# Performance work log

Hardware: AMD Instinct MI355X
Metric: run time of the kernel (lower is better)

Reference implementation:

```python
import jax, jax.numpy as jnp
import numpy as np
import math

D_MODEL, D_INNER, D_STATE, D_CONV, DT_RANK = 768, 1536, 16, 4, 48
BATCH, SEQLEN = 2, 1024
DT_MIN, DT_MAX = 1e-4, 1.0


def setup_inputs() -> dict:
    key = jax.random.key(0)
    ks = jax.random.split(key, 10)
    D, N, R, K = D_INNER, D_STATE, DT_RANK, D_CONV
    total_out = 2 * D + R + 2 * D * N

    def xavier(k, shape):
        fan_in, fan_out = shape[1], shape[0]
        a = math.sqrt(6.0 / (fan_in + fan_out))
        return jax.random.uniform(k, shape, jnp.float32, -a, a)

    x = jax.random.normal(ks[0], (BATCH, SEQLEN, D_MODEL), jnp.float32)
    W_in = xavier(ks[1], (total_out, D_MODEL))
    W_dt = xavier(ks[2], (D, R))
    W_out = xavier(ks[3], (D_MODEL, D))
    W_res = xavier(ks[4], (D, D_MODEL))
    conv_w = jax.random.normal(ks[5], (D, K), jnp.float32) * (1.0 / math.sqrt(K))
    conv_b = jnp.zeros((D,), jnp.float32)
    # A_log init: log(1..N) per inner channel
    A_log = jnp.broadcast_to(jnp.log(jnp.arange(1, N + 1, dtype=jnp.float32)), (D, N))
    Dskip = jnp.ones((D,), jnp.float32)
    # dt_bias = inverse_softplus(exp(uniform in [log dt_min, log dt_max]))
    dt = jnp.exp(jax.random.uniform(ks[6], (D,), jnp.float32) * (math.log(DT_MAX) - math.log(DT_MIN)) + math.log(DT_MIN))
    dt_bias = dt + jnp.log(-jnp.expm1(-dt))
    norm_w = jnp.ones((D,), jnp.float32)
    ln_w = jnp.ones((D_MODEL,), jnp.float32)
    ln_b = jnp.zeros((D_MODEL,), jnp.float32)
    return {
        "x": x, "ln_w": ln_w, "ln_b": ln_b, "W_in": W_in, "W_dt": W_dt,
        "conv_w": conv_w, "conv_b": conv_b, "A_log": A_log, "Dskip": Dskip,
        "dt_bias": dt_bias, "norm_w": norm_w, "W_res": W_res, "W_out": W_out,
    }


def _forward(x, ln_w, ln_b, W_in, W_dt, conv_w, conv_b, A_log, Dskip, dt_bias, norm_w, W_res, W_out):
    B, L, _ = x.shape
    D, N = A_log.shape
    K = conv_w.shape[1]
    R = W_dt.shape[1]
    # pre LayerNorm
    mu = x.mean(-1, keepdims=True)
    var = ((x - mu) ** 2).mean(-1, keepdims=True)
    xn = (x - mu) * jax.lax.rsqrt(var + 1e-5) * ln_w + ln_b
    # fused input projection, then split
    p = jnp.einsum('bld,od->blo', xn, W_in)  # (B,L,2D+R+2DN)
    z = p[..., :D]
    u = p[..., D:2 * D]
    dth = p[..., 2 * D:2 * D + R]
    Bpar = p[..., 2 * D + R:2 * D + R + D * N].reshape(B, L, D, N)
    Cpar = p[..., 2 * D + R + D * N:].reshape(B, L, D, N)
    # causal depthwise conv over time on u
    uc = jax.lax.conv_general_dilated(
        u.transpose(0, 2, 1), conv_w[:, None, :], (1,), [(K - 1, 0)],
        feature_group_count=D, dimension_numbers=('NCH', 'OIH', 'NCH'))
    u = (uc + conv_b[None, :, None]).transpose(0, 2, 1)  # (B,L,D)
    # dt: low-rank proj + bias -> softplus -> clamp
    dt = jnp.clip(jax.nn.softplus(jnp.einsum('blr,dr->bld', dth, W_dt) + dt_bias), DT_MIN, DT_MAX)
    A = -jnp.exp(A_log)  # (D,N), negative
    dA = jnp.exp(dt[..., None] * A)          # (B,L,D,N)
    dBu = (dt * u)[..., None] * Bpar         # (B,L,D,N)

    def step(h, inp):
        dA_t, dBu_t, C_t = inp               # each (B,D,N)
        h = dA_t * h + dBu_t
        return h, (C_t * h).sum(-1)          # y_t: (B,D)

    h0 = jnp.zeros((B, D, N), x.dtype)
    _, ys = jax.lax.scan(step, h0, (dA.transpose(1, 0, 2, 3),
                                    dBu.transpose(1, 0, 2, 3),
                                    Cpar.transpose(1, 0, 2, 3)))
    y = ys.transpose(1, 0, 2) + u * Dskip    # (B,L,D)
    # fused gated RMSNorm + inner residual
    res = jnp.einsum('blm,dm->bld', x, W_res)
    g = y * jax.nn.silu(z)
    g = g * jax.lax.rsqrt((g * g).mean(-1, keepdims=True) + 1e-6) * norm_w + res
    return jnp.einsum('bld,md->blm', g, W_out)


def reference(x, ln_w, ln_b, W_in, W_dt, conv_w, conv_b, A_log, Dskip, dt_bias, norm_w, W_res, W_out):
    return _forward(x, ln_w, ln_b, W_in, W_dt, conv_w, conv_b, A_log, Dskip, dt_bias, norm_w, W_res, W_out)
```

## Files before the change

### kernel.cpp

```cpp
#include <hip/hip_runtime.h>


typedef unsigned short u16;
typedef __bf16 bf16x8 __attribute__((ext_vector_type(8)));
typedef float f32x4 __attribute__((ext_vector_type(4)));

#define OPAD 52480
#define OTOT 52272
#define DI   1536
#define DM   768
#define Z0   0
#define U0   1536
#define DTH0 3072
#define B0   3120
#define C0   27696

#define SCAN_P 64
#define SCAN_T 16
#define SPF    4

#define LOG2E 1.442695040888963f

__device__ static inline u16 f2bf(float f) {
    unsigned u = __float_as_uint(f);
    u += 0x7fffu + ((u >> 16) & 1u);
    return (u16)(u >> 16);
}
__device__ static inline float bf2f(u16 s) {
    return __uint_as_float(((unsigned)s) << 16);
}

__device__ static inline void gload16(const void* g, void* l) {
    __builtin_amdgcn_global_load_lds(
        (const __attribute__((address_space(1))) unsigned int*)g,
        (__attribute__((address_space(3))) unsigned int*)l, 16, 0, 0);
}

__device__ static inline void unpack8(uint4 v, float* f) {
    unsigned w0 = v.x, w1 = v.y, w2 = v.z, w3 = v.w;
    f[0] = __uint_as_float(w0 << 16); f[1] = __uint_as_float(w0 & 0xffff0000u);
    f[2] = __uint_as_float(w1 << 16); f[3] = __uint_as_float(w1 & 0xffff0000u);
    f[4] = __uint_as_float(w2 << 16); f[5] = __uint_as_float(w2 & 0xffff0000u);
    f[6] = __uint_as_float(w3 << 16); f[7] = __uint_as_float(w3 & 0xffff0000u);
}

__device__ static inline void block_reduce2(float& a, float& b) {
    #pragma unroll
    for (int o = 32; o > 0; o >>= 1) {
        a += __shfl_down(a, o);
        b += __shfl_down(b, o);
    }
    __shared__ float sa[4], sb[4];
    int lane = threadIdx.x & 63, w = threadIdx.x >> 6;
    if (lane == 0) { sa[w] = a; sb[w] = b; }
    __syncthreads();
    a = sa[0] + sa[1] + sa[2] + sa[3];
    b = sb[0] + sb[1] + sb[2] + sb[3];
}

__global__ void __launch_bounds__(256) prep_kernel(
        const float* __restrict__ W_in, const float* __restrict__ W_res,
        const float* __restrict__ W_out, const float* __restrict__ x,
        const float* __restrict__ lnw, const float* __restrict__ lnb,
        u16* __restrict__ Wbf, u16* __restrict__ Wresbf, u16* __restrict__ Woutbf,
        u16* __restrict__ xnbf, u16* __restrict__ xbf) {
    int bid = blockIdx.x, tid = threadIdx.x;
    if (bid < 41664) {
        const float* src; u16* dst; long n_src, n_tot; long lb;
        if (bid < 39360) {
            src = W_in; dst = Wbf; n_src = (long)OTOT * DM; n_tot = (long)OPAD * DM;
            lb = bid;
        } else if (bid < 40512) {
            src = W_res; dst = Wresbf; n_src = (long)DI * DM; n_tot = n_src;
            lb = bid - 39360;
        } else {
            src = W_out; dst = Woutbf; n_src = (long)DM * DI; n_tot = n_src;
            lb = bid - 40512;
        }
        long i4 = (lb * 256 + tid) * 4;
        if (i4 >= n_tot) return;
        ushort4 o;
        if (i4 < n_src) {
            float4 v = *(const float4*)(src + i4);
            o.x = f2bf(v.x); o.y = f2bf(v.y); o.z = f2bf(v.z); o.w = f2bf(v.w);
        } else {
            o.x = o.y = o.z = o.w = 0;
        }
        *(ushort4*)(dst + i4) = o;
    } else {
        int m = bid - 41664;
        const float* xr = x + (size_t)m * DM;
        float v[3];
        v[0] = xr[tid]; v[1] = xr[tid + 256]; v[2] = xr[tid + 512];
        float s = v[0] + v[1] + v[2];
        float ss = v[0]*v[0] + v[1]*v[1] + v[2]*v[2];
        block_reduce2(s, ss);
        float mu = s * (1.f / DM);
        float var = ss * (1.f / DM) - mu * mu;
        float inv = rsqrtf(var + 1e-5f);
        #pragma unroll
        for (int i = 0; i < 3; ++i) {
            int d = tid + i * 256;
            float xn = (v[i] - mu) * inv * lnw[d] + lnb[d];
            xnbf[(size_t)m * DM + d] = f2bf(xn);
            xbf[(size_t)m * DM + d] = f2bf(v[i]);
        }
    }
}

template <int OUT_BF16, int ATOMIC>
__global__ void __launch_bounds__(256) gemm_bt(const u16* __restrict__ A,
        const u16* __restrict__ B, void* __restrict__ C, int K, int ldk, int ldc) {
    __shared__ u16 smem[2 * 128 * 64];
    u16* As = smem;
    u16* Bs = smem + 128 * 64;
    int tid = threadIdx.x;
    int m0 = blockIdx.x * 128, n0 = blockIdx.y * 128;
    int lane = tid & 63, wave = tid >> 6;
    int wm = wave >> 1, wn = wave & 1;
    int l15 = lane & 15, l4 = lane >> 4;
    f32x4 acc[4][4] = {};
    const u16* Ag = A + (size_t)m0 * ldk + (size_t)blockIdx.z * K;
    const u16* Bg = B + (size_t)n0 * ldk + (size_t)blockIdx.z * K;
    int crow = tid >> 3;
    int ccol = ((tid & 7) ^ ((tid >> 3) & 7)) * 8;
    int ldsoff = (tid & 192) * 16;
    int xr = l15 & 7;

    for (int k0 = 0; k0 < K; k0 += 64) {
        __syncthreads();
        #pragma unroll
        for (int it = 0; it < 4; ++it) {
            gload16(Ag + (size_t)(it * 32 + crow) * ldk + k0 + ccol,
                    (char*)As + it * 4096 + ldsoff);
            gload16(Bg + (size_t)(it * 32 + crow) * ldk + k0 + ccol,
                    (char*)Bs + it * 4096 + ldsoff);
        }
        __syncthreads();
        const u16* Arow = As + (wm * 64 + l15) * 64;
        const u16* Brow = Bs + (wn * 64 + l15) * 64;
        #pragma unroll
        for (int kk8 = 0; kk8 < 8; kk8 += 4) {
            int sw = ((l4 + kk8) ^ xr) * 8;
            bf16x8 af[4], bfr[4];
            #pragma unroll
            for (int i = 0; i < 4; ++i) af[i] = *(const bf16x8*)(Arow + i * 16 * 64 + sw);
            #pragma unroll
            for (int j = 0; j < 4; ++j) bfr[j] = *(const bf16x8*)(Brow + j * 16 * 64 + sw);
            #pragma unroll
            for (int i = 0; i < 4; ++i)
                #pragma unroll
                for (int j = 0; j < 4; ++j)
                    acc[i][j] = __builtin_amdgcn_mfma_f32_16x16x32_bf16(
                        af[i], bfr[j], acc[i][j], 0, 0, 0);
        }
    }
    #pragma unroll
    for (int i = 0; i < 4; ++i) {
        int row = m0 + wm * 64 + i * 16 + l4 * 4;
        #pragma unroll
        for (int j = 0; j < 4; ++j) {
            int col = n0 + wn * 64 + j * 16 + l15;
            #pragma unroll
            for (int r = 0; r < 4; ++r) {
                size_t off = (size_t)(row + r) * ldc + col;
                if (ATOMIC)        atomicAdd((float*)C + off, acc[i][j][r]);
                else if (OUT_BF16) ((u16*)C)[off] = f2bf(acc[i][j][r]);
                else               ((float*)C)[off] = acc[i][j][r];
            }
        }
    }
}

#define G2_BUF  65536
#define G2_HALF 16384
#define G2_BOFF 32768

__global__ void __launch_bounds__(512, 2) gemm256_bt(const u16* __restrict__ A,
        const u16* __restrict__ B, u16* __restrict__ C, int K, int ldc) {
    __shared__ u16 smem[65536];
    char* smemc = (char*)smem;
    const int tid = threadIdx.x;
    const int l = tid & 63, w = tid >> 6;
    const int wm = w >> 2, wn = w & 3;
    const int l15 = l & 15, l4 = l >> 4;
    const int flat = blockIdx.y * 8 + blockIdx.x;
    const int wg = (flat & 7) * 205 + (flat >> 3);
    const int m0 = (wg & 7) * 256, n0 = (wg >> 3) * 256;
    const int NT = K >> 6;

    const int rA = l15 >> 1;
    const int rdoff = rA * 128 + ((((l4 << 1) + (l15 & 1)) ^ ((rA & 3) << 1)) << 4);
    const int wpr = (l & 7) ^ (((l >> 3) & 3) << 1);
    const int srow = w * 32 + ((l >> 3) << 1) + (wpr & 1);
    const u16* Ast = A + (size_t)(m0 + srow) * K + (wpr >> 1) * 8;
    const u16* Bst = B + (size_t)(n0 + srow) * K + (wpr >> 1) * 8;
    const int sdst = w * 2048;

    f32x4 acc[8][4] = {};
    bf16x8 bvK[4];

#define G2_STAGE(MATP, MOFF, nxt, sh, tk)                                      \
    gload16(MATP + (size_t)(tk) * 64 + (sh) * 32,                              \
            smemc + (nxt) * G2_BUF + (MOFF) + (sh) * G2_HALF + sdst);          \
    gload16(MATP + (size_t)16 * K + (size_t)(tk) * 64 + (sh) * 32,             \
            smemc + (nxt) * G2_BUF + (MOFF) + (sh) * G2_HALF + sdst + 1024);

#define G2_PHASE(cur, nxt, rh, h, READB, SMAT, SMOFF, sh, tk, DO_VM)           \
    {                                                                          \
        G2_STAGE(SMAT, SMOFF, nxt, sh, tk);                                    \
        const char* Ab = smemc + (cur) * G2_BUF + (h) * G2_HALF                \
                         + (wm * 128 + (rh) * 64) * 64 + rdoff;                \
        bf16x8 af[4];                                                          \
        if (READB) {                                                           \
            const char* Bb = smemc + (cur) * G2_BUF + G2_BOFF + (h) * G2_HALF  \
                             + (wn * 64) * 64 + rdoff;                         \
            _Pragma("unroll")                                                  \
            for (int j = 0; j < 4; ++j)                                        \
                bvK[j] = *(const bf16x8*)(Bb + j * 1024);                      \
        }                                                                      \
        _Pragma("unroll")                                                      \
        for (int i = 0; i < 4; ++i) af[i] = *(const bf16x8*)(Ab + i * 1024);   \
        __builtin_amdgcn_s_barrier();                                          \
        __builtin_amdgcn_s_setprio(1);                                         \
        _Pragma("unroll")                                                      \
        for (int i = 0; i < 4; ++i)                                            \
            _Pragma("unroll")                                                  \
            for (int j = 0; j < 4; ++j)                                        \
                acc[(rh) * 4 + i][j] = __builtin_amdgcn_mfma_f32_16x16x32_bf16(\
                    af[i], bvK[j], acc[(rh) * 4 + i][j], 0, 0, 0);             \
        __builtin_amdgcn_s_setprio(0);                                         \
        if (DO_VM) asm volatile("s_waitcnt vmcnt(4)" ::: "memory");            \
        __builtin_amdgcn_s_barrier();                                          \
    }

#define G2_TILE(cur, nxt, tk)                                                  \
    G2_PHASE(cur, nxt, 0, 0, 1, Ast, 0,       0, tk, 0)                        \
    G2_PHASE(cur, nxt, 1, 0, 0, Bst, G2_BOFF, 0, tk, 1)                        \
    G2_PHASE(cur, nxt, 0, 1, 1, Ast, 0,       1, tk, 0)                        \
    G2_PHASE(cur, nxt, 1, 1, 0, Bst, G2_BOFF, 1, tk, 1)

    G2_STAGE(Ast, 0,       0, 0, 0);
    G2_STAGE(Bst, G2_BOFF, 0, 0, 0);
    G2_STAGE(Ast, 0,       0, 1, 0);
    G2_STAGE(Bst, G2_BOFF, 0, 1, 0);
    asm volatile("s_waitcnt vmcnt(4)" ::: "memory");
    __builtin_amdgcn_s_barrier();

    for (int t = 0; t < NT; t += 2) {
        int tk1 = t + 1;
        int tk2 = (t + 2 < NT) ? t + 2 : NT - 1;
        G2_TILE(0, 1, tk1)
        G2_TILE(1, 0, tk2)
    }

    #pragma unroll
    for (int ai = 0; ai < 8; ++ai) {
        int row = m0 + wm * 128 + ai * 16 + l4 * 4;
        #pragma unroll
        for (int j = 0; j < 4; ++j) {
            int col = n0 + wn * 64 + j * 16 + l15;
            #pragma unroll
            for (int r = 0; r < 4; ++r)
                C[(size_t)(row + r) * ldc + col] = f2bf(acc[ai][j][r]);
        }
    }
#undef G2_STAGE
#undef G2_PHASE
#undef G2_TILE
}

__global__ void __launch_bounds__(256) dt_kernel(const u16* __restrict__ p,
        const float* __restrict__ Wdt, const float* __restrict__ dt_bias,
        float* __restrict__ dt) {
    int m0 = blockIdx.x * 4, tid = threadIdx.x;
    __shared__ float dth_s[4 * 48];
    for (int i = tid; i < 4 * 48; i += 256)
        dth_s[i] = bf2f(p[(size_t)(m0 + i / 48) * OPAD + DTH0 + (i % 48)]);
    __syncthreads();
    #pragma unroll
    for (int ii = 0; ii < 6; ++ii) {
        int d = ii * 256 + tid;
        float base = dt_bias[d];
        float acc[4];
        #pragma unroll
        for (int mm = 0; mm < 4; ++mm) acc[mm] = base;
        for (int r = 0; r < 48; ++r) {
            float wv = Wdt[d * 48 + r];
            #pragma unroll
            for (int mm = 0; mm < 4; ++mm)
                acc[mm] = fmaf(wv, dth_s[mm * 48 + r], acc[mm]);
        }
        #pragma unroll
        for (int mm = 0; mm < 4; ++mm) {
            float xv = acc[mm];
            float sp = xv > 20.f ? xv : log1pf(__expf(xv));
            sp = fminf(fmaxf(sp, 1e-4f), 1.0f);
            dt[(size_t)(m0 + mm) * DI + d] = sp;
        }
    }
}

__global__ void __launch_bounds__(256, 2) scan1_kernel(const u16* __restrict__ p,
        const float* __restrict__ dt, const float* __restrict__ A_log,
        const float* __restrict__ cw, const float* __restrict__ cb,
        float* __restrict__ chkA, float* __restrict__ chkB) {
    int d = blockIdx.x * 256 + threadIdx.x;
    int b = blockIdx.y, c = blockIdx.z;
    int t0base = c * SCAN_T;
    float a[16];
    #pragma unroll
    for (int n = 0; n < 16; ++n) a[n] = -__expf(A_log[d * 16 + n]) * LOG2E;
    float cw0 = cw[d*4], cw1 = cw[d*4+1], cw2 = cw[d*4+2], cw3 = cw[d*4+3];
    float cbv = cb[d];
    const u16* pB = p + (size_t)(b * 1024 + t0base) * OPAD + B0 + d * 16;
    const u16* pU = p + (size_t)(b * 1024 + t0base) * OPAD + U0 + d;
    const float* dtp = dt + (size_t)(b * 1024 + t0base) * DI + d;
    float x1, x2, x3;
    if (c == 0) { x1 = x2 = x3 = 0.f; }
    else {
        x1 = bf2f(*(pU - (long)OPAD));
        x2 = bf2f(*(pU - 2L * OPAD));
        x3 = bf2f(*(pU - 3L * OPAD));
    }
    uint4 Br[SPF][2]; float dtr[SPF], xur[SPF];
    #pragma unroll
    for (int i = 0; i < SPF; ++i) {
        Br[i][0] = *(const uint4*)(pB + (size_t)i * OPAD);
        Br[i][1] = *(const uint4*)(pB + (size_t)i * OPAD + 8);
        dtr[i] = dtp[(size_t)i * DI];
        xur[i] = bf2f(pU[(size_t)i * OPAD]);
    }
    float h[16], Av[16];
    #pragma unroll
    for (int n = 0; n < 16; ++n) { h[n] = 0.f; Av[n] = 1.f; }
    for (int t0 = 0; t0 < SCAN_T; t0 += SPF) {
        #pragma unroll
        for (int s = 0; s < SPF; ++s) {
            int t = t0 + s;
            uint4 b0 = Br[s][0], b1 = Br[s][1];
            float dtv = dtr[s], xt = xur[s];
            int tl = t + SPF < SCAN_T ? t + SPF : SCAN_T - 1;
            Br[s][0] = *(const uint4*)(pB + (size_t)tl * OPAD);
            Br[s][1] = *(const uint4*)(pB + (size_t)tl * OPAD + 8);
            dtr[s] = dtp[(size_t)tl * DI];
            xur[s] = bf2f(pU[(size_t)tl * OPAD]);
            float uv = cbv;
            uv = fmaf(cw0, x3, uv);
            uv = fmaf(cw1, x2, uv);
            uv = fmaf(cw2, x1, uv);
            uv = fmaf(cw3, xt, uv);
            x3 = x2; x2 = x1; x1 = xt;
            float Bf[16];
            unpack8(b0, Bf); unpack8(b1, Bf + 8);
            float dtu = dtv * uv;
            #pragma unroll
            for (int n = 0; n < 16; ++n) {
                float dA = exp2f(dtv * a[n]);
                h[n] = fmaf(dA, h[n], dtu * Bf[n]);
                Av[n] *= dA;
            }
        }
    }
    size_t o = (((size_t)c * 2 + b) * 1536 + d) * 16;
    #pragma unroll
    for (int k = 0; k < 4; ++k) {
        *(float4*)(chkA + o + k * 4) = make_float4(Av[4*k], Av[4*k+1], Av[4*k+2], Av[4*k+3]);
        *(float4*)(chkB + o + k * 4) = make_float4(h[4*k], h[4*k+1], h[4*k+2], h[4*k+3]);
    }
}

__global__ void __launch_bounds__(256) scan_comb_kernel(const float* __restrict__ chkA,
        const float* __restrict__ chkB, float* __restrict__ hstart) {
    int idx = blockIdx.x * 256 + threadIdx.x;
    float hs = 0.f;
    for (int c = 0; c < SCAN_P; ++c) {
        size_t o = (size_t)c * 49152 + idx;
        hstart[o] = hs;
        hs = fmaf(chkA[o], hs, chkB[o]);
    }
}

__global__ void __launch_bounds__(256, 2) scan2_kernel(const u16* __restrict__ p,
        const float* __restrict__ dt, const float* __restrict__ A_log,
        const float* __restrict__ cw, const float* __restrict__ cb,
        const float* __restrict__ Dskip,
        const float* __restrict__ hstart, float* __restrict__ y) {
    int d = blockIdx.x * 256 + threadIdx.x;
    int b = blockIdx.y, c = blockIdx.z;
    int t0base = c * SCAN_T;
    float a[16];
    #pragma unroll
    for (int n = 0; n < 16; ++n) a[n] = -__expf(A_log[d * 16 + n]) * LOG2E;
    float Dsk = Dskip[d];
    float cw0 = cw[d*4], cw1 = cw[d*4+1], cw2 = cw[d*4+2], cw3 = cw[d*4+3];
    float cbv = cb[d];
    const u16* pB = p + (size_t)(b * 1024 + t0base) * OPAD + B0 + d * 16;
    const u16* pC = p + (size_t)(b * 1024 + t0base) * OPAD + C0 + d * 16;
    const u16* pU = p + (size_t)(b * 1024 + t0base) * OPAD + U0 + d;
    const float* dtp = dt + (size_t)(b * 1024 + t0base) * DI + d;
    float* yp        = y  + (size_t)(b * 1024 + t0base) * DI + d;
    float x1, x2, x3;
    if (c == 0) { x1 = x2 = x3 = 0.f; }
    else {
        x1 = bf2f(*(pU - (long)OPAD));
        x2 = bf2f(*(pU - 2L * OPAD));
        x3 = bf2f(*(pU - 3L * OPAD));
    }
    uint4 Br[SPF][2], Cr[SPF][2]; float dtr[SPF], xur[SPF];
    #pragma unroll
    for (int i = 0; i < SPF; ++i) {
        Br[i][0] = *(const uint4*)(pB + (size_t)i * OPAD);
        Br[i][1] = *(const uint4*)(pB + (size_t)i * OPAD + 8);
        Cr[i][0] = *(const uint4*)(pC + (size_t)i * OPAD);
        Cr[i][1] = *(const uint4*)(pC + (size_t)i * OPAD + 8);
        dtr[i] = dtp[(size_t)i * DI];
        xur[i] = bf2f(pU[(size_t)i * OPAD]);
    }
    float h[16];
    {
        size_t o = ((size_t)c * 3072 + (size_t)b * 1536 + d) * 16;
        #pragma unroll
        for (int k = 0; k < 4; ++k) {
            float4 hv = *(const float4*)(hstart + o + k * 4);
            h[4*k] = hv.x; h[4*k+1] = hv.y; h[4*k+2] = hv.z; h[4*k+3] = hv.w;
        }
    }
    for (int t0 = 0; t0 < SCAN_T; t0 += SPF) {
        #pragma unroll
        for (int s = 0; s < SPF; ++s) {
            int t = t0 + s;
            uint4 b0 = Br[s][0], b1 = Br[s][1], c0 = Cr[s][0], c1 = Cr[s][1];
            float dtv = dtr[s], xt = xur[s];
            int tl = t + SPF < SCAN_T ? t + SPF : SCAN_T - 1;
            Br[s][0] = *(const uint4*)(pB + (size_t)tl * OPAD);
            Br[s][1] = *(const uint4*)(pB + (size_t)tl * OPAD + 8);
            Cr[s][0] = *(const uint4*)(pC + (size_t)tl * OPAD);
            Cr[s][1] = *(const uint4*)(pC + (size_t)tl * OPAD + 8);
            dtr[s] = dtp[(size_t)tl * DI];
            xur[s] = bf2f(pU[(size_t)tl * OPAD]);
            float uv = cbv;
            uv = fmaf(cw0, x3, uv);
            uv = fmaf(cw1, x2, uv);
            uv = fmaf(cw2, x1, uv);
            uv = fmaf(cw3, xt, uv);
            x3 = x2; x2 = x1; x1 = xt;
            float Bf[16], Cf[16];
            unpack8(b0, Bf); unpack8(b1, Bf + 8);
            unpack8(c0, Cf); unpack8(c1, Cf + 8);
            float dtu = dtv * uv;
            #pragma unroll
            for (int n = 0; n < 16; ++n) {
                float dA = exp2f(dtv * a[n]);
                h[n] = fmaf(dA, h[n], dtu * Bf[n]);
            }
            float a0 = fmaf(Cf[0], h[0], uv * Dsk), a1 = Cf[1] * h[1];
            float a2 = Cf[2] * h[2], a3 = Cf[3] * h[3];
            #pragma unroll
            for (int n = 4; n < 16; n += 4) {
                a0 = fmaf(Cf[n],   h[n],   a0);
                a1 = fmaf(Cf[n+1], h[n+1], a1);
                a2 = fmaf(Cf[n+2], h[n+2], a2);
                a3 = fmaf(Cf[n+3], h[n+3], a3);
            }
            yp[(size_t)t * DI] = (a0 + a1) + (a2 + a3);
        }
    }
}

__global__ void __launch_bounds__(256) gate_kernel(const u16* __restrict__ p,
        const float* __restrict__ y, const float* __restrict__ res,
        const float* __restrict__ norm_w, u16* __restrict__ g) {
    int m = blockIdx.x, tid = threadIdx.x;
    const u16* pz = p + (size_t)m * OPAD + Z0;
    const float* yr = y + (size_t)m * DI;
    float gp[6];
    float ss = 0.f, dummy = 0.f;
    #pragma unroll
    for (int i = 0; i < 6; ++i) {
        int d = i * 256 + tid;
        float z = bf2f(pz[d]);
        float gv = yr[d] * z / (1.f + __expf(-z));
        gp[i] = gv;
        ss += gv * gv;
    }
    block_reduce2(ss, dummy);
    float scale = rsqrtf(ss * (1.f / DI) + 1e-6f);
    #pragma unroll
    for (int i = 0; i < 6; ++i) {
        int d = i * 256 + tid;
        float val = gp[i] * scale * norm_w[d] + res[(size_t)m * DI + d];
        g[(size_t)m * DI + d] = f2bf(val);
    }
}

extern "C" void kernel_launch(void* const* d_in, const int* in_sizes, int n_in,
                              void* d_out, int out_size, void* d_ws, size_t ws_size,
                              hipStream_t stream) {
    const float* x       = (const float*)d_in[0];
    const float* ln_w    = (const float*)d_in[1];
    const float* ln_b    = (const float*)d_in[2];
    const float* W_in    = (const float*)d_in[3];
    const float* W_dt    = (const float*)d_in[4];
    const float* conv_w  = (const float*)d_in[5];
    const float* conv_b  = (const float*)d_in[6];
    const float* A_log   = (const float*)d_in[7];
    const float* Dskip   = (const float*)d_in[8];
    const float* dt_bias = (const float*)d_in[9];
    const float* norm_w  = (const float*)d_in[10];
    const float* W_res   = (const float*)d_in[11];
    const float* W_out   = (const float*)d_in[12];
    float* out = (float*)d_out;

    char* wsb = (char*)d_ws;
    u16* Wbf     = (u16*)(wsb + 0);
    u16* Wresbf  = (u16*)(wsb + 80609280);
    u16* Woutbf  = (u16*)(wsb + 82968576);
    u16* xnbf    = (u16*)(wsb + 85327872);
    u16* xbf     = (u16*)(wsb + 88473600);
    u16* pbuf    = (u16*)(wsb + 91619328);
    float* dtv   = (float*)(wsb + 319160320);
    float* ybuf  = (float*)(wsb + 331743232);
    float* resb  = (float*)(wsb + 344326144);
    u16* gbuf    = (u16*)(wsb + 356909056);
    float* chkA  = (float*)(wsb + 0);
    float* chkB  = (float*)(wsb + 12582912);
    float* hst   = (float*)(wsb + 25165824);

    prep_kernel<<<43712, 256, 0, stream>>>(W_in, W_res, W_out, x, ln_w, ln_b,
                                           Wbf, Wresbf, Woutbf, xnbf, xbf);
    gemm256_bt<<<dim3(8, 205), 512, 0, stream>>>(xnbf, Wbf, pbuf, DM, OPAD);
    hipMemsetAsync(resb, 0, 12582912, stream);
    gemm_bt<0, 1><<<dim3(16, 12, 2), 256, 0, stream>>>(xbf, Wresbf, resb, 384, DM, DI);
    dt_kernel<<<512, 256, 0, stream>>>(pbuf, W_dt, dt_bias, dtv);
    scan1_kernel<<<dim3(6, 2, SCAN_P), 256, 0, stream>>>(pbuf, dtv, A_log, conv_w, conv_b, chkA, chkB);
    scan_comb_kernel<<<192, 256, 0, stream>>>(chkA, chkB, hst);
    scan2_kernel<<<dim3(6, 2, SCAN_P), 256, 0, stream>>>(pbuf, dtv, A_log, conv_w, conv_b, Dskip, hst, ybuf);
    gate_kernel<<<2048, 256, 0, stream>>>(pbuf, ybuf, resb, norm_w, gbuf);
    hipMemsetAsync(out, 0, (size_t)2048 * DM * 4, stream);
    gemm_bt<0, 1><<<dim3(16, 6, 4), 256, 0, stream>>>(gbuf, Woutbf, out, 384, DI, DM);
}
```

Before: 693.9 us.

## Fuse residual GEMM into main projection launch and drop split-K atomics

The residual projection x·W_res now runs as extra workgroups appended to the big input-projection GEMM launch. Each of these 512-thread blocks holds two independent 128x128 tiles over the full K=768 and stores fp32 directly, so the memset and atomic split-K path go away. The output projection also drops split-K: it runs 96 blocks over the full K with plain stores, removing a memset and the atomics. The cost is fewer blocks and therefore less parallelism on the output GEMM, plus uneven work inside the fused launch.

```diff
diff --git a/kernel.cpp b/kernel.cpp
--- a/kernel.cpp
+++ b/kernel.cpp
@@ -108,9 +108,9 @@
     }
 }
 
-template <int OUT_BF16, int ATOMIC>
+template <int OUT_BF16>
 __global__ void __launch_bounds__(256) gemm_bt(const u16* __restrict__ A,
-        const u16* __restrict__ B, void* __restrict__ C, int K, int ldk, int ldc) {
+        const u16* __restrict__ B, void* __restrict__ C, int K, int ldc) {
     __shared__ u16 smem[2 * 128 * 64];
     u16* As = smem;
     u16* Bs = smem + 128 * 64;
@@ -120,8 +120,8 @@
     int wm = wave >> 1, wn = wave & 1;
     int l15 = lane & 15, l4 = lane >> 4;
     f32x4 acc[4][4] = {};
-    const u16* Ag = A + (size_t)m0 * ldk + (size_t)blockIdx.z * K;
-    const u16* Bg = B + (size_t)n0 * ldk + (size_t)blockIdx.z * K;
+    const u16* Ag = A + (size_t)m0 * K;
+    const u16* Bg = B + (size_t)n0 * K;
     int crow = tid >> 3;
     int ccol = ((tid & 7) ^ ((tid >> 3) & 7)) * 8;
     int ldsoff = (tid & 192) * 16;
@@ -131,9 +131,9 @@
         __syncthreads();
         #pragma unroll
         for (int it = 0; it < 4; ++it) {
-            gload16(Ag + (size_t)(it * 32 + crow) * ldk + k0 + ccol,
+            gload16(Ag + (size_t)(it * 32 + crow) * K + k0 + ccol,
                     (char*)As + it * 4096 + ldsoff);
-            gload16(Bg + (size_t)(it * 32 + crow) * ldk + k0 + ccol,
+            gload16(Bg + (size_t)(it * 32 + crow) * K + k0 + ccol,
                     (char*)Bs + it * 4096 + ldsoff);
         }
         __syncthreads();
@@ -164,9 +164,8 @@
             #pragma unroll
             for (int r = 0; r < 4; ++r) {
                 size_t off = (size_t)(row + r) * ldc + col;
-                if (ATOMIC)        atomicAdd((float*)C + off, acc[i][j][r]);
-                else if (OUT_BF16) ((u16*)C)[off] = f2bf(acc[i][j][r]);
-                else               ((float*)C)[off] = acc[i][j][r];
+                if (OUT_BF16) ((u16*)C)[off] = f2bf(acc[i][j][r]);
+                else          ((float*)C)[off] = acc[i][j][r];
             }
         }
     }
@@ -177,28 +176,32 @@
 #define G2_BOFF 32768
 
 __global__ void __launch_bounds__(512, 2) gemm256_bt(const u16* __restrict__ A,
-        const u16* __restrict__ B, u16* __restrict__ C, int K, int ldc) {
+        const u16* __restrict__ B, u16* __restrict__ C, int K, int ldc,
+        const u16* __restrict__ Ares, const u16* __restrict__ Bres,
+        float* __restrict__ Cres) {
     __shared__ u16 smem[65536];
     char* smemc = (char*)smem;
     const int tid = threadIdx.x;
-    const int l = tid & 63, w = tid >> 6;
-    const int wm = w >> 2, wn = w & 3;
-    const int l15 = l & 15, l4 = l >> 4;
-    const int flat = blockIdx.y * 8 + blockIdx.x;
-    const int wg = (flat & 7) * 205 + (flat >> 3);
-    const int m0 = (wg & 7) * 256, n0 = (wg >> 3) * 256;
-    const int NT = K >> 6;
-
-    const int rA = l15 >> 1;
-    const int rdoff = rA * 128 + ((((l4 << 1) + (l15 & 1)) ^ ((rA & 3) << 1)) << 4);
-    const int wpr = (l & 7) ^ (((l >> 3) & 3) << 1);
-    const int srow = w * 32 + ((l >> 3) << 1) + (wpr & 1);
-    const u16* Ast = A + (size_t)(m0 + srow) * K + (wpr >> 1) * 8;
-    const u16* Bst = B + (size_t)(n0 + srow) * K + (wpr >> 1) * 8;
-    const int sdst = w * 2048;
-
-    f32x4 acc[8][4] = {};
-    bf16x8 bvK[4];
+    const int flat = blockIdx.x;
+
+    if (flat < 1640) {
+        const int l = tid & 63, w = tid >> 6;
+        const int wm = w >> 2, wn = w & 3;
+        const int l15 = l & 15, l4 = l >> 4;
+        const int wg = (flat & 7) * 205 + (flat >> 3);
+        const int m0 = (wg & 7) * 256, n0 = (wg >> 3) * 256;
+        const int NT = K >> 6;
+
+        const int rA = l15 >> 1;
+        const int rdoff = rA * 128 + ((((l4 << 1) + (l15 & 1)) ^ ((rA & 3) << 1)) << 4);
+        const int wpr = (l & 7) ^ (((l >> 3) & 3) << 1);
+        const int srow = w * 32 + ((l >> 3) << 1) + (wpr & 1);
+        const u16* Ast = A + (size_t)(m0 + srow) * K + (wpr >> 1) * 8;
+        const u16* Bst = B + (size_t)(n0 + srow) * K + (wpr >> 1) * 8;
+        const int sdst = w * 2048;
+
+        f32x4 acc[8][4] = {};
+        bf16x8 bvK[4];
 
 #define G2_STAGE(MATP, MOFF, nxt, sh, tk)                                      \
     gload16(MATP + (size_t)(tk) * 64 + (sh) * 32,                              \
@@ -240,34 +243,92 @@
     G2_PHASE(cur, nxt, 0, 1, 1, Ast, 0,       1, tk, 0)                        \
     G2_PHASE(cur, nxt, 1, 1, 0, Bst, G2_BOFF, 1, tk, 1)
 
-    G2_STAGE(Ast, 0,       0, 0, 0);
-    G2_STAGE(Bst, G2_BOFF, 0, 0, 0);
-    G2_STAGE(Ast, 0,       0, 1, 0);
-    G2_STAGE(Bst, G2_BOFF, 0, 1, 0);
-    asm volatile("s_waitcnt vmcnt(4)" ::: "memory");
-    __builtin_amdgcn_s_barrier();
-
-    for (int t = 0; t < NT; t += 2) {
-        int tk1 = t + 1;
-        int tk2 = (t + 2 < NT) ? t + 2 : NT - 1;
-        G2_TILE(0, 1, tk1)
-        G2_TILE(1, 0, tk2)
-    }
-
-    #pragma unroll
-    for (int ai = 0; ai < 8; ++ai) {
-        int row = m0 + wm * 128 + ai * 16 + l4 * 4;
-        #pragma unroll
-        for (int j = 0; j < 4; ++j) {
-            int col = n0 + wn * 64 + j * 16 + l15;
-            #pragma unroll
-            for (int r = 0; r < 4; ++r)
-                C[(size_t)(row + r) * ldc + col] = f2bf(acc[ai][j][r]);
-        }
-    }
+        G2_STAGE(Ast, 0,       0, 0, 0);
+        G2_STAGE(Bst, G2_BOFF, 0, 0, 0);
+        G2_STAGE(Ast, 0,       0, 1, 0);
+        G2_STAGE(Bst, G2_BOFF, 0, 1, 0);
+        asm volatile("s_waitcnt vmcnt(4)" ::: "memory");
+        __builtin_amdgcn_s_barrier();
+
+        for (int t = 0; t < NT; t += 2) {
+            int tk1 = t + 1;
+            int tk2 = (t + 2 < NT) ? t + 2 : NT - 1;
+            G2_TILE(0, 1, tk1)
+            G2_TILE(1, 0, tk2)
+        }
+
+        #pragma unroll
+        for (int ai = 0; ai < 8; ++ai) {
+            int row = m0 + wm * 128 + ai * 16 + l4 * 4;
+            #pragma unroll
+            for (int j = 0; j < 4; ++j) {
+                int col = n0 + wn * 64 + j * 16 + l15;
+                #pragma unroll
+                for (int r = 0; r < 4; ++r)
+                    C[(size_t)(row + r) * ldc + col] = f2bf(acc[ai][j][r]);
+            }
+        }
 #undef G2_STAGE
 #undef G2_PHASE
 #undef G2_TILE
+    } else {
+        const int half = tid >> 8;
+        const int tid2 = tid & 255;
+        const int t2 = (flat - 1640) * 2 + half;
+        const int m0 = (t2 & 15) * 128, n0 = (t2 >> 4) * 128;
+        u16* As = smem + half * 16384;
+        u16* Bs = As + 8192;
+        int lane = tid2 & 63, wave = tid2 >> 6;
+        int wm = wave >> 1, wn = wave & 1;
+        int l15 = lane & 15, l4 = lane >> 4;
+        f32x4 acc[4][4] = {};
+        const u16* Ag = Ares + (size_t)m0 * DM;
+        const u16* Bg = Bres + (size_t)n0 * DM;
+        int crow = tid2 >> 3;
+        int ccol = ((tid2 & 7) ^ ((tid2 >> 3) & 7)) * 8;
+        int ldsoff = (tid2 & 192) * 16;
+        int xr = l15 & 7;
+
+        for (int k0 = 0; k0 < DM; k0 += 64) {
+            __syncthreads();
+            #pragma unroll
+            for (int it = 0; it < 4; ++it) {
+                gload16(Ag + (size_t)(it * 32 + crow) * DM + k0 + ccol,
+                        (char*)As + it * 4096 + ldsoff);
+                gload16(Bg + (size_t)(it * 32 + crow) * DM + k0 + ccol,
+                        (char*)Bs + it * 4096 + ldsoff);
+            }
+            __syncthreads();
+            const u16* Arow = As + (wm * 64 + l15) * 64;
+            const u16* Brow = Bs + (wn * 64 + l15) * 64;
+            #pragma unroll
+            for (int kk8 = 0; kk8 < 8; kk8 += 4) {
+                int sw = ((l4 + kk8) ^ xr) * 8;
+                bf16x8 af[4], bfr[4];
+                #pragma unroll
+                for (int i = 0; i < 4; ++i) af[i] = *(const bf16x8*)(Arow + i * 16 * 64 + sw);
+                #pragma unroll
+                for (int j = 0; j < 4; ++j) bfr[j] = *(const bf16x8*)(Brow + j * 16 * 64 + sw);
+                #pragma unroll
+                for (int i = 0; i < 4; ++i)
+                    #pragma unroll
+                    for (int j = 0; j < 4; ++j)
+                        acc[i][j] = __builtin_amdgcn_mfma_f32_16x16x32_bf16(
+                            af[i], bfr[j], acc[i][j], 0, 0, 0);
+            }
+        }
+        #pragma unroll
+        for (int i = 0; i < 4; ++i) {
+            int row = m0 + wm * 64 + i * 16 + l4 * 4;
+            #pragma unroll
+            for (int j = 0; j < 4; ++j) {
+                int col = n0 + wn * 64 + j * 16 + l15;
+                #pragma unroll
+                for (int r = 0; r < 4; ++r)
+                    Cres[(size_t)(row + r) * DI + col] = acc[i][j][r];
+            }
+        }
+    }
 }
 
 __global__ void __launch_bounds__(256) dt_kernel(const u16* __restrict__ p,
@@ -529,14 +590,12 @@
 
     prep_kernel<<<43712, 256, 0, stream>>>(W_in, W_res, W_out, x, ln_w, ln_b,
                                            Wbf, Wresbf, Woutbf, xnbf, xbf);
-    gemm256_bt<<<dim3(8, 205), 512, 0, stream>>>(xnbf, Wbf, pbuf, DM, OPAD);
-    hipMemsetAsync(resb, 0, 12582912, stream);
-    gemm_bt<0, 1><<<dim3(16, 12, 2), 256, 0, stream>>>(xbf, Wresbf, resb, 384, DM, DI);
+    gemm256_bt<<<1736, 512, 0, stream>>>(xnbf, Wbf, pbuf, DM, OPAD,
+                                         xbf, Wresbf, resb);
     dt_kernel<<<512, 256, 0, stream>>>(pbuf, W_dt, dt_bias, dtv);
     scan1_kernel<<<dim3(6, 2, SCAN_P), 256, 0, stream>>>(pbuf, dtv, A_log, conv_w, conv_b, chkA, chkB);
     scan_comb_kernel<<<192, 256, 0, stream>>>(chkA, chkB, hst);
     scan2_kernel<<<dim3(6, 2, SCAN_P), 256, 0, stream>>>(pbuf, dtv, A_log, conv_w, conv_b, Dskip, hst, ybuf);
     gate_kernel<<<2048, 256, 0, stream>>>(pbuf, ybuf, resb, norm_w, gbuf);
-    hipMemsetAsync(out, 0, (size_t)2048 * DM * 4, stream);
-    gemm_bt<0, 1><<<dim3(16, 6, 4), 256, 0, stream>>>(gbuf, Woutbf, out, 384, DI, DM);
-}
+    gemm_bt<0><<<dim3(16, 6), 256, 0, stream>>>(gbuf, Woutbf, out, DI, DM);
+}
```

New measurement: 673.6 us. -2.9%, faster.
